# Performance work log

Measured on AMD Instinct MI355X. Metric: run time of the kernel, lower is better.

Reference implementation:

```python
import jax, jax.numpy as jnp
import numpy as np

NUM_HEADS = 16
HEAD_DIM = 64  # hidden_size // num_heads


def _logsparse_allowed(seq_len):
    # allowed[i, j] True if key j is attended by query i:
    # j == i, j == i-1, or j == i - 2^k (k >= 1); combined with causal (j <= i).
    i = jnp.arange(seq_len)[:, None]
    j = jnp.arange(seq_len)[None, :]
    diff = i - j
    pow2 = (diff > 0) & ((diff & (diff - 1)) == 0)  # covers diff==1 and diff==2^k
    return (diff == 0) | pow2  # implies diff >= 0, so causal is subsumed


def setup_inputs() -> dict:
    key = jax.random.key(0)
    ks = jax.random.split(key, 7)
    B, S, H = 4, 2048, 1024
    return {
        "hidden_states": jax.random.normal(ks[0], (B, S, H), dtype=jnp.float32),
        "attention_mask": jnp.zeros((B, 1, 1, S), dtype=jnp.float32),
        "Wq": jax.random.normal(ks[1], (H, H), dtype=jnp.float32) * 0.02,
        "bq": jnp.zeros((H,), dtype=jnp.float32),
        "Wk": jax.random.normal(ks[2], (H, H), dtype=jnp.float32) * 0.02,
        "bk": jnp.zeros((H,), dtype=jnp.float32),
        "Wv": jax.random.normal(ks[3], (H, H), dtype=jnp.float32) * 0.02,
        "bv": jnp.zeros((H,), dtype=jnp.float32),
    }


def _split_heads(x):
    B, S, _ = x.shape
    return x.reshape(B, S, NUM_HEADS, HEAD_DIM).transpose(0, 2, 1, 3)  # b h t d


def reference(hidden_states, attention_mask, Wq, bq, Wk, bk, Wv, bv):
    B, S, H = hidden_states.shape
    q = _split_heads(hidden_states @ Wq.T + bq)
    k = _split_heads(hidden_states @ Wk.T + bk)
    v = _split_heads(hidden_states @ Wv.T + bv)

    scores = jnp.einsum("bhqd,bhkd->bhqk", q, k) * (HEAD_DIM ** -0.5)
    allowed = _logsparse_allowed(S)  # [S, S] bool
    scores = jnp.where(allowed[None, None], scores, -jnp.inf)
    scores = scores + attention_mask  # [B,1,1,S] additive mask
    probs = jax.nn.softmax(scores, axis=-1)
    out = jnp.einsum("bhqk,bhkd->bhqd", probs, v)
    return out.transpose(0, 2, 1, 3).reshape(B, S, H)
```

## Files before the change

### kernel.cpp

```cpp
#include <hip/hip_runtime.h>
#include <hip/hip_bf16.h>

#define S_LEN   2048
#define NHEADS  16
#define HDIM    64
#define HID     1024
#define BATCH   4
#define M_ROWS  (BATCH * S_LEN)

#define BM 128
#define BN 128
#define BK 64

typedef __attribute__((ext_vector_type(8))) short short8;
typedef __attribute__((ext_vector_type(4))) float floatx4;
typedef __attribute__((ext_vector_type(4))) unsigned short ushort4v;

__device__ __forceinline__ unsigned short f2bf_rne(float x) {
  union { float f; unsigned u; } v; v.f = x;
  unsigned r = v.u + 0x7fffu + ((v.u >> 16) & 1u);
  return (unsigned short)(r >> 16);
}

__device__ __forceinline__ float bf2f(unsigned short u) {
  union { unsigned u; float f; } c; c.u = ((unsigned)u) << 16;
  return c.f;
}

__device__ __forceinline__ void glds16(const unsigned short* g, unsigned short* l) {
  __builtin_amdgcn_global_load_lds(
      (const __attribute__((address_space(1))) unsigned int*)g,
      (__attribute__((address_space(3))) unsigned int*)l, 16, 0, 0);
}

#define HS4 (M_ROWS * HID / 4)
#define W4  (HID * HID / 4)
__global__ __launch_bounds__(256) void cast_all(
    const float* __restrict__ hs, const float* __restrict__ Wq,
    const float* __restrict__ Wk, const float* __restrict__ Wv,
    unsigned short* __restrict__ hsb, unsigned short* __restrict__ wqb,
    unsigned short* __restrict__ wkb, unsigned short* __restrict__ wvb) {
  int idx = blockIdx.x * 256 + threadIdx.x;
  const float* in;
  unsigned short* out;
  int off;
  if (idx < HS4) {
    in = hs; out = hsb; off = idx;
  } else {
    int r = idx - HS4;
    int seg = r >> 18;
    off = r & (W4 - 1);
    in  = (seg == 0) ? Wq  : (seg == 1) ? Wk  : Wv;
    out = (seg == 0) ? wqb : (seg == 1) ? wkb : wvb;
  }
  floatx4 v = __builtin_nontemporal_load((const floatx4*)in + off);
  ushort4v o;
  o.x = f2bf_rne(v.x);
  o.y = f2bf_rne(v.y);
  o.z = f2bf_rne(v.z);
  o.w = f2bf_rne(v.w);
  ((ushort4v*)out)[off] = o;
}

__global__ __launch_bounds__(256) void qkv_gemm(
    const unsigned short* __restrict__ A,
    const unsigned short* __restrict__ W0, const unsigned short* __restrict__ W1,
    const unsigned short* __restrict__ W2,
    const float* __restrict__ b0, const float* __restrict__ b1,
    const float* __restrict__ b2,
    unsigned short* __restrict__ O0, unsigned short* __restrict__ O1,
    unsigned short* __restrict__ O2) {
  const int K = HID;
  const int N = HID;
  const int z = blockIdx.z;
  const unsigned short* __restrict__ W = (z == 0) ? W0 : (z == 1) ? W1 : W2;
  const float* __restrict__ bias = (z == 0) ? b0 : (z == 1) ? b1 : b2;
  unsigned short* __restrict__ O = (z == 0) ? O0 : (z == 1) ? O1 : O2;

  __shared__ __align__(16) unsigned short As[BM * BK];
  __shared__ __align__(16) unsigned short Bs[BN * BK];

  const int tid = threadIdx.x;
  const int w = tid >> 6;
  const int lane = tid & 63;
  const int m0 = blockIdx.x * BM;
  const int n0 = blockIdx.y * BN;

  const int lr = lane >> 3;
  const int cc = (lane & 7) ^ lr;
  const unsigned short* gA[4];
  const unsigned short* gB[4];
  unsigned short* lA[4];
  unsigned short* lB[4];
  #pragma unroll
  for (int u = 0; u < 4; ++u) {
    const int seg = w * 4 + u;
    const int r = seg * 8 + lr;
    gA[u] = A + (size_t)(m0 + r) * K + cc * 8;
    gB[u] = W + (size_t)(n0 + r) * K + cc * 8;
    lA[u] = As + seg * 512;
    lB[u] = Bs + seg * 512;
  }

  const int lrow = lane & 15;
  const int qd = lane >> 4;
  const int sw = lrow & 7;
  const int arow = (w & 1) * 64 + lrow;
  const int brow = (w >> 1) * 64 + lrow;

  floatx4 acc[4][4] = {};

  for (int k0 = 0; k0 < K; k0 += BK) {
    #pragma unroll
    for (int u = 0; u < 4; ++u) {
      glds16(gA[u] + k0, lA[u]);
      glds16(gB[u] + k0, lB[u]);
    }
    __syncthreads();

    #pragma unroll
    for (int kk = 0; kk < 2; ++kk) {
      const int cp = (((kk << 2) | qd) ^ sw) * 8;
      short8 af[4], bf[4];
      #pragma unroll
      for (int im = 0; im < 4; ++im)
        af[im] = *(const short8*)(As + (arow + im * 16) * BK + cp);
      #pragma unroll
      for (int in = 0; in < 4; ++in)
        bf[in] = *(const short8*)(Bs + (brow + in * 16) * BK + cp);

      #pragma unroll
      for (int im = 0; im < 4; ++im)
        #pragma unroll
        for (int in = 0; in < 4; ++in)
          acc[im][in] = __builtin_amdgcn_mfma_f32_16x16x32_bf16(af[im], bf[in], acc[im][in], 0, 0, 0);
    }
    __syncthreads();
  }

  #pragma unroll
  for (int im = 0; im < 4; ++im) {
    #pragma unroll
    for (int in = 0; in < 4; ++in) {
      const int col = n0 + (w >> 1) * 64 + in * 16 + lrow;
      const float bb = bias[col];
      #pragma unroll
      for (int r = 0; r < 4; ++r) {
        const int row = m0 + (w & 1) * 64 + im * 16 + (qd << 2) + r;
        O[(size_t)row * N + col] = f2bf_rne(acc[im][in][r] + bb);
      }
    }
  }
}

__global__ __launch_bounds__(256) void logsparse_attn(
    const unsigned short* __restrict__ Q, const unsigned short* __restrict__ K,
    const unsigned short* __restrict__ V, const float* __restrict__ mask,
    float* __restrict__ out) {
  const int bid = (blockIdx.x & 7) * 512 + (blockIdx.x >> 3);
  const int tid = threadIdx.x;
  const int l = tid & 7;
  const int qglob = bid * 32 + (tid >> 3);

  const int i = qglob & (S_LEN - 1);
  const int h = (qglob >> 11) & (NHEADS - 1);
  const int b = qglob >> 15;

  const size_t base = (size_t)b * S_LEN * HID + h * HDIM + l * 8;

  int js[12];
  js[0] = i;
  int nj = 1;
  for (int d = 1; d <= i; d <<= 1) js[nj++] = i - d;
  #pragma unroll
  for (int t = 0; t < 12; ++t)
    if (t >= nj) js[t] = i;

  short8 k8[12];
  #pragma unroll
  for (int t = 0; t < 12; ++t)
    k8[t] = *(const short8*)(K + base + (size_t)js[t] * HID);
  const short8 q8 = *(const short8*)(Q + base + (size_t)i * HID);
  float mk[12];
  #pragma unroll
  for (int t = 0; t < 12; ++t)
    mk[t] = mask[b * S_LEN + js[t]];

  float qf[8];
  #pragma unroll
  for (int e = 0; e < 8; ++e) qf[e] = bf2f((unsigned short)q8[e]);

  float s[12];
  #pragma unroll
  for (int t = 0; t < 12; ++t) {
    float p = 0.f;
    #pragma unroll
    for (int e = 0; e < 8; ++e) p += qf[e] * bf2f((unsigned short)k8[t][e]);
    p += __shfl_xor(p, 1, 64);
    p += __shfl_xor(p, 2, 64);
    p += __shfl_xor(p, 4, 64);
    s[t] = (t < nj) ? (p * 0.125f + mk[t]) : -1e30f;
  }

  float mx = s[0];
  #pragma unroll
  for (int t = 1; t < 12; ++t) mx = fmaxf(mx, s[t]);
  float lsum = 0.f;
  #pragma unroll
  for (int t = 0; t < 12; ++t) { s[t] = __expf(s[t] - mx); lsum += s[t]; }
  const float inv = 1.f / lsum;

  short8 v8[12];
  #pragma unroll
  for (int t = 0; t < 12; ++t)
    v8[t] = *(const short8*)(V + base + (size_t)js[t] * HID);

  float o[8] = {};
  #pragma unroll
  for (int t = 0; t < 12; ++t) {
    #pragma unroll
    for (int e = 0; e < 8; ++e) o[e] += s[t] * bf2f((unsigned short)v8[t][e]);
  }

  float* op = out + base + (size_t)i * HID;
  floatx4 o0 = {o[0] * inv, o[1] * inv, o[2] * inv, o[3] * inv};
  floatx4 o1 = {o[4] * inv, o[5] * inv, o[6] * inv, o[7] * inv};
  __builtin_nontemporal_store(o0, (floatx4*)op);
  __builtin_nontemporal_store(o1, (floatx4*)(op + 4));
}

extern "C" void kernel_launch(void* const* d_in, const int* in_sizes, int n_in,
                              void* d_out, int out_size, void* d_ws, size_t ws_size,
                              hipStream_t stream) {
  const float* hs   = (const float*)d_in[0];
  const float* mask = (const float*)d_in[1];
  const float* Wq   = (const float*)d_in[2];
  const float* bq   = (const float*)d_in[3];
  const float* Wk   = (const float*)d_in[4];
  const float* bk   = (const float*)d_in[5];
  const float* Wv   = (const float*)d_in[6];
  const float* bv   = (const float*)d_in[7];
  float* out = (float*)d_out;

  unsigned short* hsb = (unsigned short*)d_ws;
  unsigned short* wqb = hsb + (size_t)M_ROWS * HID;
  unsigned short* wkb = wqb + (size_t)HID * HID;
  unsigned short* wvb = wkb + (size_t)HID * HID;
  unsigned short* Qb = wvb + (size_t)HID * HID;
  unsigned short* Kb = Qb + (size_t)M_ROWS * HID;
  unsigned short* Vb = Kb + (size_t)M_ROWS * HID;

  {
    int quads = HS4 + 3 * W4;
    cast_all<<<quads / 256, 256, 0, stream>>>(hs, Wq, Wk, Wv, hsb, wqb, wkb, wvb);
  }

  {
    dim3 grid(M_ROWS / BM, HID / BN, 3);
    qkv_gemm<<<grid, 256, 0, stream>>>(hsb, wqb, wkb, wvb, bq, bk, bv, Qb, Kb, Vb);
  }

  {
    int blocks = (BATCH * NHEADS * S_LEN) / 32;
    logsparse_attn<<<blocks, 256, 0, stream>>>(Qb, Kb, Vb, mask, out);
  }
}
```

Baseline: 181.3 us.

## Triple-buffer QKV GEMM with 256x128 tiles, 512 threads and XCD-aware block mapping

```diff
diff --git a/kernel.cpp b/kernel.cpp
--- a/kernel.cpp
+++ b/kernel.cpp
@@ -7,10 +7,6 @@
 #define HID     1024
 #define BATCH   4
 #define M_ROWS  (BATCH * S_LEN)
-
-#define BM 128
-#define BN 128
-#define BK 64
 
 typedef __attribute__((ext_vector_type(8))) short short8;
 typedef __attribute__((ext_vector_type(4))) float floatx4;
@@ -62,7 +58,7 @@
   ((ushort4v*)out)[off] = o;
 }
 
-__global__ __launch_bounds__(256) void qkv_gemm(
+__global__ __launch_bounds__(512, 2) void qkv_gemm(
     const unsigned short* __restrict__ A,
     const unsigned short* __restrict__ W0, const unsigned short* __restrict__ W1,
     const unsigned short* __restrict__ W2,
@@ -72,81 +68,104 @@
     unsigned short* __restrict__ O2) {
   const int K = HID;
   const int N = HID;
-  const int z = blockIdx.z;
-  const unsigned short* __restrict__ W = (z == 0) ? W0 : (z == 1) ? W1 : W2;
-  const float* __restrict__ bias = (z == 0) ? b0 : (z == 1) ? b1 : b2;
-  unsigned short* __restrict__ O = (z == 0) ? O0 : (z == 1) ? O1 : O2;
-
-  __shared__ __align__(16) unsigned short As[BM * BK];
-  __shared__ __align__(16) unsigned short Bs[BN * BK];
+
+  __shared__ __align__(16) unsigned short lds[3 * 24576];
 
   const int tid = threadIdx.x;
   const int w = tid >> 6;
   const int lane = tid & 63;
-  const int m0 = blockIdx.x * BM;
-  const int n0 = blockIdx.y * BN;
+
+  const int bid = blockIdx.x;
+  const int lid = (bid & 7) * 96 + (bid >> 3);
+  const int mi   = lid & 31;
+  const int slab = lid >> 5;
+  const int ni = slab & 7;
+  const int z  = slab >> 3;
+  const int m0 = mi << 8;
+  const int n0 = ni << 7;
+
+  const unsigned short* __restrict__ Wz = (z == 0) ? W0 : (z == 1) ? W1 : W2;
+  const float* __restrict__ bias = (z == 0) ? b0 : (z == 1) ? b1 : b2;
+  unsigned short* __restrict__ O = (z == 0) ? O0 : (z == 1) ? O1 : O2;
 
   const int lr = lane >> 3;
-  const int cc = (lane & 7) ^ lr;
-  const unsigned short* gA[4];
-  const unsigned short* gB[4];
-  unsigned short* lA[4];
-  unsigned short* lB[4];
-  #pragma unroll
-  for (int u = 0; u < 4; ++u) {
-    const int seg = w * 4 + u;
-    const int r = seg * 8 + lr;
-    gA[u] = A + (size_t)(m0 + r) * K + cc * 8;
-    gB[u] = W + (size_t)(n0 + r) * K + cc * 8;
-    lA[u] = As + seg * 512;
-    lB[u] = Bs + seg * 512;
-  }
+  const int ccs = (lane & 7) ^ lr;
+  const unsigned short* gsrc[6];
+  unsigned short* ldst[6];
+  #pragma unroll
+  for (int u = 0; u < 6; ++u) {
+    const int seg = w * 6 + u;
+    if (seg < 32) {
+      gsrc[u] = A + (size_t)(m0 + seg * 8 + lr) * K + ccs * 8;
+      ldst[u] = lds + seg * 512;
+    } else {
+      gsrc[u] = Wz + (size_t)(n0 + (seg - 32) * 8 + lr) * K + ccs * 8;
+      ldst[u] = lds + 16384 + (seg - 32) * 512;
+    }
+  }
+
+  auto stage3 = [&](int t, int h) {
+    const int bofs = (t % 3) * 24576;
+    const int ko = t * 64;
+    #pragma unroll
+    for (int u = h * 3; u < h * 3 + 3; ++u)
+      glds16(gsrc[u] + ko, ldst[u] + bofs);
+  };
 
   const int lrow = lane & 15;
   const int qd = lane >> 4;
   const int sw = lrow & 7;
-  const int arow = (w & 1) * 64 + lrow;
-  const int brow = (w >> 1) * 64 + lrow;
+  const int wm = w & 3;
+  const int wn = w >> 2;
+  const int arow = wm * 64 + lrow;
+  const int brow = wn * 64 + lrow;
 
   floatx4 acc[4][4] = {};
 
-  for (int k0 = 0; k0 < K; k0 += BK) {
-    #pragma unroll
-    for (int u = 0; u < 4; ++u) {
-      glds16(gA[u] + k0, lA[u]);
-      glds16(gB[u] + k0, lB[u]);
-    }
-    __syncthreads();
+  stage3(0, 0); stage3(0, 1);
+  stage3(1, 0); stage3(1, 1);
+
+  for (int t = 0; t < 16; ++t) {
+    asm volatile("s_waitcnt lgkmcnt(0)" ::: "memory");
+    if (t < 15) asm volatile("s_waitcnt vmcnt(6)" ::: "memory");
+    else        asm volatile("s_waitcnt vmcnt(0)" ::: "memory");
+    __builtin_amdgcn_s_barrier();
+    asm volatile("" ::: "memory");
+
+    const unsigned short* Asb = lds + (t % 3) * 24576;
+    const unsigned short* Bsb = Asb + 16384;
+    const bool pf = (t + 2 < 16);
 
     #pragma unroll
     for (int kk = 0; kk < 2; ++kk) {
-      const int cp = (((kk << 2) | qd) ^ sw) * 8;
+      if (pf) stage3(t + 2, kk);
+      const int cp = (((kk << 2) | qd) ^ sw) << 3;
       short8 af[4], bf[4];
       #pragma unroll
       for (int im = 0; im < 4; ++im)
-        af[im] = *(const short8*)(As + (arow + im * 16) * BK + cp);
+        af[im] = *(const short8*)(Asb + (arow + im * 16) * 64 + cp);
       #pragma unroll
       for (int in = 0; in < 4; ++in)
-        bf[in] = *(const short8*)(Bs + (brow + in * 16) * BK + cp);
-
+        bf[in] = *(const short8*)(Bsb + (brow + in * 16) * 64 + cp);
+      __builtin_amdgcn_s_setprio(1);
       #pragma unroll
       for (int im = 0; im < 4; ++im)
         #pragma unroll
         for (int in = 0; in < 4; ++in)
           acc[im][in] = __builtin_amdgcn_mfma_f32_16x16x32_bf16(af[im], bf[in], acc[im][in], 0, 0, 0);
+      __builtin_amdgcn_s_setprio(0);
     }
-    __syncthreads();
   }
 
   #pragma unroll
   for (int im = 0; im < 4; ++im) {
     #pragma unroll
     for (int in = 0; in < 4; ++in) {
-      const int col = n0 + (w >> 1) * 64 + in * 16 + lrow;
+      const int col = n0 + wn * 64 + in * 16 + lrow;
       const float bb = bias[col];
       #pragma unroll
       for (int r = 0; r < 4; ++r) {
-        const int row = m0 + (w & 1) * 64 + im * 16 + (qd << 2) + r;
+        const int row = m0 + wm * 64 + im * 16 + (qd << 2) + r;
         O[(size_t)row * N + col] = f2bf_rne(acc[im][in][r] + bb);
       }
     }
@@ -256,8 +275,7 @@
   }
 
   {
-    dim3 grid(M_ROWS / BM, HID / BN, 3);
-    qkv_gemm<<<grid, 256, 0, stream>>>(hsb, wqb, wkb, wvb, bq, bk, bv, Qb, Kb, Vb);
+    qkv_gemm<<<768, 512, 0, stream>>>(hsb, wqb, wkb, wvb, bq, bk, bv, Qb, Kb, Vb);
   }
 
   {
```

Result: slower. 192.7 us (+6.3%).
